# Kernel tuning notes

Hardware: AMD Instinct MI355X
Metric: run time of the kernel (lower is better)

## Reference

```python
import jax, jax.numpy as jnp
import numpy as np

V = 25   # NTU joints
NE = 5   # number of hyper-edge types


def setup_inputs() -> dict:
    key = jax.random.key(0)
    ks = jax.random.split(key, 8)
    N, C, T = 64, 12, 300
    x = jax.random.normal(ks[0], (N, C, T, V), dtype=jnp.float32)
    # binary incidence matrices [V, E] with E == V, as in the NTU hyper-edge tables
    hs = [jax.random.bernoulli(ks[1 + i], 0.2, (V, V)).astype(jnp.float32) for i in range(NE)]
    in_ch, out_ch = 3, 64
    w_mlp = jax.random.normal(ks[6], (out_ch, in_ch * NE), dtype=jnp.float32) * (1.0 / np.sqrt(in_ch * NE))
    b_mlp = jnp.zeros((out_ch,), dtype=jnp.float32)
    return {"x": x, "h_local": hs[0], "h_center": hs[1], "h_figl": hs[2],
            "h_figr": hs[3], "h_hand": hs[4], "w_mlp": w_mlp, "b_mlp": b_mlp}


def _normalized_aggregate(w, h):
    # w: [N, T, E], h: [V, E] (E == V)
    degree_v = jnp.einsum('ve,bte->btv', h, w)
    # pow(d, -0.5): inf at d==0 and nan at d<0 are both zeroed in the original
    dv_pos = degree_v > 0
    degree_v = jnp.where(dv_pos, jax.lax.rsqrt(jnp.where(dv_pos, degree_v, 1.0)), 0.0)
    degree_e = jnp.sum(h, axis=0)                      # [E]
    de_nz = degree_e != 0
    degree_e = jnp.where(de_nz, 1.0 / jnp.where(de_nz, degree_e, 1.0), 0.0)
    # fused dh * w * degree_e chain: [N, T, V, E]
    dhwb = degree_v[..., None] * h[None, None] * w[:, :, None, :] * degree_e
    dhwbht = jnp.einsum('btve,ue->btvu', dhwb, h)      # [N, T, V, V]
    return dhwbht * degree_v[:, :, None, :]


def reference(x, h_local, h_center, h_figl, h_figr, h_hand, w_mlp, b_mlp):
    ws = (x[:, 6], x[:, 7], x[:, 9], x[:, 10], x[:, 11])
    hs = (h_local, h_center, h_figl, h_figr, h_hand)
    hwh_cat = jnp.concatenate([_normalized_aggregate(w, h) for w, h in zip(ws, hs)], axis=-2)  # [N,T,5V,V]
    feat = x[:, :3]                                    # [N, 3, T, V]
    N, C, T, Vv = feat.shape
    support = jnp.einsum('btvu,bctu->bctv', hwh_cat, feat)          # [N, C, T, 5V]
    support = support.reshape(N, C, T, NE, Vv).transpose(0, 3, 1, 2, 4).reshape(N, NE * C, T, Vv)
    out = jnp.einsum('oi,bitv->botv', w_mlp, support) + b_mlp[None, :, None, None]
    return jax.nn.relu(out)
```

## Files before the change

### kernel.cpp

```cpp
#include <hip/hip_runtime.h>

#define NE  5
#define V   25
#define NT  300
#define NC  12
#define CO  64
#define WPB 4
#define GX  38

typedef float f4 __attribute__((ext_vector_type(4)));
typedef float f2 __attribute__((ext_vector_type(2)));

#define WSYNC() do { asm volatile("s_waitcnt lgkmcnt(0)" ::: "memory"); \
                     __builtin_amdgcn_sched_barrier(0); } while (0)

__device__ __forceinline__ float hsel(unsigned m, int e, float w) {
    int s = ((int)(m << (31 - e))) >> 31;
    return __int_as_float(__float_as_int(w) & s);
}

#define OW   0
#define ODV  224
#define OG   364
#define OB   504
#define OFP  924
#define OST  1344
#define SCRF 2344

__global__ __launch_bounds__(256, 4) void hyper_main(
    const float* __restrict__ x,
    const float* __restrict__ h0, const float* __restrict__ h1,
    const float* __restrict__ h2, const float* __restrict__ h3,
    const float* __restrict__ h4,
    const float* __restrict__ wmlp, const float* __restrict__ bmlp,
    float* __restrict__ out)
{
    __shared__ unsigned RM[125];
    __shared__ unsigned CM[125];
    __shared__ float    DE[125];
    __shared__ __align__(16) float SCR[WPB][SCRF];

    const int tid  = threadIdx.x;
    const int lane = tid & 63;
    const int wid  = tid >> 6;
    const int b    = blockIdx.y;

    if (tid < 125) {
        int i = tid / 25, v = tid % 25;
        const float* hp = (i==0)?h0:(i==1)?h1:(i==2)?h2:(i==3)?h3:h4;
        unsigned m = 0;
        for (int e = 0; e < V; ++e) if (hp[v*V + e] != 0.f) m |= (1u << e);
        RM[tid] = m;
    } else if (tid < 250) {
        int idx = tid - 125, i = idx / 25, e = idx % 25;
        const float* hp = (i==0)?h0:(i==1)?h1:(i==2)?h2:(i==3)?h3:h4;
        unsigned m = 0; float s = 0.f;
        for (int u = 0; u < V; ++u) {
            float hv = hp[u*V + e];
            s += hv;
            if (hv != 0.f) m |= (1u << u);
        }
        CM[idx] = m;
        DE[idx] = (s != 0.f) ? __fdiv_rn(1.f, s) : 0.f;
    }
    __syncthreads();

    const int pp = blockIdx.x * WPB + wid;
    if (pp >= NT/2) return;

    float* S = SCR[wid];

    const float* xb[4]; int lo[4];
    {
        #pragma unroll
        for (int r = 0; r < 4; ++r) {
            int q  = r*64 + lane;
            int qq = (q < 200) ? q : 0;
            int ch = qq / 25, e = qq % 25;
            int xc = (ch < 5) ? (ch + 6 + (ch >= 2 ? 1 : 0)) : (ch - 5);
            lo[r] = OW + ch*28 + e;
            xb[r] = x + (size_t)(b*NC + xc)*NT*V + e;
        }
    }
    const bool act3 = (lane < 8);

    float pf0, pf1, pf2, pf3;
    {
        int t0 = 2 * pp;
        pf0 = xb[0][t0*V]; pf1 = xb[1][t0*V];
        pf2 = xb[2][t0*V]; pf3 = xb[3][t0*V];
    }

    for (int tp = 0; tp < 2; ++tp) {

        S[lo[0]] = pf0; S[lo[1]] = pf1; S[lo[2]] = pf2;
        if (act3) S[lo[3]] = pf3;
        WSYNC();

        if (tp == 0) {
            int tn = 2*pp + 1;
            pf0 = xb[0][tn*V]; pf1 = xb[1][tn*V];
            pf2 = xb[2][tn*V]; pf3 = xb[3][tn*V];
        }

        for (int r = 0; r < 2; ++r) {
            int idx = r*64 + lane;
            if (idx < 125) {
                int i = idx / 25, v = idx % 25;
                unsigned m = RM[idx];
                const float* wi = S + OW + i*28;
                f4 w0 = *(const f4*)(wi+0),  w1 = *(const f4*)(wi+4),
                   w2 = *(const f4*)(wi+8),  w3 = *(const f4*)(wi+12),
                   w4 = *(const f4*)(wi+16), w5 = *(const f4*)(wi+20),
                   w6 = *(const f4*)(wi+24);
                float L0 = 0.f, L1 = 0.f, L2 = 0.f, L3 = 0.f;
                L0=__fadd_rn(L0,hsel(m, 0,w0.x)); L1=__fadd_rn(L1,hsel(m, 1,w0.y));
                L2=__fadd_rn(L2,hsel(m, 2,w0.z)); L3=__fadd_rn(L3,hsel(m, 3,w0.w));
                L0=__fadd_rn(L0,hsel(m, 4,w1.x)); L1=__fadd_rn(L1,hsel(m, 5,w1.y));
                L2=__fadd_rn(L2,hsel(m, 6,w1.z)); L3=__fadd_rn(L3,hsel(m, 7,w1.w));
                L0=__fadd_rn(L0,hsel(m, 8,w2.x)); L1=__fadd_rn(L1,hsel(m, 9,w2.y));
                L2=__fadd_rn(L2,hsel(m,10,w2.z)); L3=__fadd_rn(L3,hsel(m,11,w2.w));
                L0=__fadd_rn(L0,hsel(m,12,w3.x)); L1=__fadd_rn(L1,hsel(m,13,w3.y));
                L2=__fadd_rn(L2,hsel(m,14,w3.z)); L3=__fadd_rn(L3,hsel(m,15,w3.w));
                L0=__fadd_rn(L0,hsel(m,16,w4.x)); L1=__fadd_rn(L1,hsel(m,17,w4.y));
                L2=__fadd_rn(L2,hsel(m,18,w4.z)); L3=__fadd_rn(L3,hsel(m,19,w4.w));
                L0=__fadd_rn(L0,hsel(m,20,w5.x)); L1=__fadd_rn(L1,hsel(m,21,w5.y));
                L2=__fadd_rn(L2,hsel(m,22,w5.z)); L3=__fadd_rn(L3,hsel(m,23,w5.w));
                float s = __fadd_rn(__fadd_rn(L0,L1), __fadd_rn(L2,L3));
                s = __fadd_rn(s, hsel(m, 24, w6.x));
                float dvv = (s > 0.f) ? (float)(1.0 / sqrt((double)s)) : 0.f;
                S[ODV + i*28 + v] = dvv;
                S[OG  + i*28 + v] = S[OW + i*28 + v] * DE[idx];
                float f0 = S[OW + 5*28 + v];
                float f1 = S[OW + 6*28 + v];
                float f2v = S[OW + 7*28 + v];
                S[OB + (0*5+i)*28 + v] = dvv * f0;
                S[OB + (1*5+i)*28 + v] = dvv * f1;
                S[OB + (2*5+i)*28 + v] = dvv * f2v;
            }
        }
        WSYNC();

        for (int r = 0; r < 2; ++r) {
            int idx = r*64 + lane;
            if (idx < 125) {
                int i = idx / 25, e = idx % 25;
                unsigned m = CM[idx];
                const float* bp = S + OB + i*28;
                float a0 = 0.f, a1 = 0.f, a2 = 0.f;
                while (m) {
                    int u = __builtin_ctz(m); m &= m - 1;
                    a0 += bp[u]; a1 += bp[140 + u]; a2 += bp[280 + u];
                }
                float gg = S[OG + i*28 + e];
                S[OFP + (i*3+0)*28 + e] = a0 * gg;
                S[OFP + (i*3+1)*28 + e] = a1 * gg;
                S[OFP + (i*3+2)*28 + e] = a2 * gg;
            }
        }
        WSYNC();

        for (int r = 0; r < 2; ++r) {
            int idx = r*64 + lane;
            if (idx < 125) {
                int i = idx / 25, v = idx % 25;
                unsigned m = RM[idx];
                const float* fp = S + OFP + i*3*28;
                float a0 = 0.f, a1 = 0.f, a2 = 0.f;
                while (m) {
                    int e = __builtin_ctz(m); m &= m - 1;
                    a0 += fp[e]; a1 += fp[28 + e]; a2 += fp[56 + e];
                }
                float dd = S[ODV + i*28 + v];
                float* st = S + OST + (tp*25 + v)*20 + i*3;
                st[0] = a0 * dd; st[1] = a1 * dd; st[2] = a2 * dd;
            }
        }
        WSYNC();
    }

    if (lane < 50) {
        const float* st = S + OST + lane*20;
        f4 s0 = *(const f4*)(st+0), s1 = *(const f4*)(st+4),
           s2 = *(const f4*)(st+8), s3 = *(const f4*)(st+12);
        s3.w = 0.f;
        float* ob = out + (size_t)b*CO*7500 + (size_t)pp*50 + lane;
        #pragma unroll 2
        for (int o2 = 0; o2 < 32; ++o2) {
            int o = 2*o2;
            const float* wa = wmlp + o*15;
            const float* wb = wa + 15;
            f2 a = (f2){bmlp[o], bmlp[o+1]};
            a += (f2){wa[ 0], wb[ 0]} * s0.x;
            a += (f2){wa[ 1], wb[ 1]} * s0.y;
            a += (f2){wa[ 2], wb[ 2]} * s0.z;
            a += (f2){wa[ 3], wb[ 3]} * s0.w;
            a += (f2){wa[ 4], wb[ 4]} * s1.x;
            a += (f2){wa[ 5], wb[ 5]} * s1.y;
            a += (f2){wa[ 6], wb[ 6]} * s1.z;
            a += (f2){wa[ 7], wb[ 7]} * s1.w;
            a += (f2){wa[ 8], wb[ 8]} * s2.x;
            a += (f2){wa[ 9], wb[ 9]} * s2.y;
            a += (f2){wa[10], wb[10]} * s2.z;
            a += (f2){wa[11], wb[11]} * s2.w;
            a += (f2){wa[12], wb[12]} * s3.x;
            a += (f2){wa[13], wb[13]} * s3.y;
            a += (f2){wa[14], wb[14]} * s3.z;
            __builtin_nontemporal_store(fmaxf(a.x, 0.f), ob + (size_t)o*7500);
            __builtin_nontemporal_store(fmaxf(a.y, 0.f), ob + (size_t)(o+1)*7500);
        }
    }
}

extern "C" void kernel_launch(void* const* d_in, const int* in_sizes, int n_in,
                              void* d_out, int out_size, void* d_ws, size_t ws_size,
                              hipStream_t stream) {
    const float* x    = (const float*)d_in[0];
    const float* h0   = (const float*)d_in[1];
    const float* h1   = (const float*)d_in[2];
    const float* h2   = (const float*)d_in[3];
    const float* h3   = (const float*)d_in[4];
    const float* h4   = (const float*)d_in[5];
    const float* wmlp = (const float*)d_in[6];
    const float* bmlp = (const float*)d_in[7];
    float* out = (float*)d_out;

    hyper_main<<<dim3(GX, 64, 1), dim3(256,1,1), 0, stream>>>(
        x, h0, h1, h2, h3, h4, wmlp, bmlp, out);
}
```

Before: 76.16 us.

## Process both timesteps of a wave together in one pass

Each wave now loads both timesteps' inputs up front and runs each aggregation stage once over 250 work items, instead of looping twice over 125 items. This halves the number of in-wave LDS sync points and fills nearly all lanes in each stage iteration. The separate gated-weight buffer is dropped: that product is recomputed where it is needed. The scratch layout now lets the output staging area alias regions that are dead by then, and the per-wave scratch grows slightly. The trade-off is that the software prefetch overlap between timesteps is lost, and the larger LDS footprint may affect occupancy.

```diff
diff --git a/kernel.cpp b/kernel.cpp
--- a/kernel.cpp
+++ b/kernel.cpp
@@ -19,13 +19,12 @@
     return __int_as_float(__float_as_int(w) & s);
 }
 
-#define OW   0
-#define ODV  224
-#define OG   364
-#define OB   504
-#define OFP  924
-#define OST  1344
-#define SCRF 2344
+#define ODV  0
+#define OFP  280
+#define OWB  1120
+#define OBB  1568
+#define OST  1408
+#define SCRF 2408
 
 __global__ __launch_bounds__(256, 4) void hyper_main(
     const float* __restrict__ x,
@@ -70,114 +69,103 @@
 
     float* S = SCR[wid];
 
-    const float* xb[4]; int lo[4];
-    {
-        #pragma unroll
-        for (int r = 0; r < 4; ++r) {
-            int q  = r*64 + lane;
-            int qq = (q < 200) ? q : 0;
-            int ch = qq / 25, e = qq % 25;
-            int xc = (ch < 5) ? (ch + 6 + (ch >= 2 ? 1 : 0)) : (ch - 5);
-            lo[r] = OW + ch*28 + e;
-            xb[r] = x + (size_t)(b*NC + xc)*NT*V + e;
-        }
-    }
-    const bool act3 = (lane < 8);
-
-    float pf0, pf1, pf2, pf3;
-    {
-        int t0 = 2 * pp;
-        pf0 = xb[0][t0*V]; pf1 = xb[1][t0*V];
-        pf2 = xb[2][t0*V]; pf3 = xb[3][t0*V];
-    }
-
-    for (int tp = 0; tp < 2; ++tp) {
-
-        S[lo[0]] = pf0; S[lo[1]] = pf1; S[lo[2]] = pf2;
-        if (act3) S[lo[3]] = pf3;
-        WSYNC();
-
-        if (tp == 0) {
-            int tn = 2*pp + 1;
-            pf0 = xb[0][tn*V]; pf1 = xb[1][tn*V];
-            pf2 = xb[2][tn*V]; pf3 = xb[3][tn*V];
-        }
-
-        for (int r = 0; r < 2; ++r) {
-            int idx = r*64 + lane;
-            if (idx < 125) {
-                int i = idx / 25, v = idx % 25;
-                unsigned m = RM[idx];
-                const float* wi = S + OW + i*28;
-                f4 w0 = *(const f4*)(wi+0),  w1 = *(const f4*)(wi+4),
-                   w2 = *(const f4*)(wi+8),  w3 = *(const f4*)(wi+12),
-                   w4 = *(const f4*)(wi+16), w5 = *(const f4*)(wi+20),
-                   w6 = *(const f4*)(wi+24);
-                float L0 = 0.f, L1 = 0.f, L2 = 0.f, L3 = 0.f;
-                L0=__fadd_rn(L0,hsel(m, 0,w0.x)); L1=__fadd_rn(L1,hsel(m, 1,w0.y));
-                L2=__fadd_rn(L2,hsel(m, 2,w0.z)); L3=__fadd_rn(L3,hsel(m, 3,w0.w));
-                L0=__fadd_rn(L0,hsel(m, 4,w1.x)); L1=__fadd_rn(L1,hsel(m, 5,w1.y));
-                L2=__fadd_rn(L2,hsel(m, 6,w1.z)); L3=__fadd_rn(L3,hsel(m, 7,w1.w));
-                L0=__fadd_rn(L0,hsel(m, 8,w2.x)); L1=__fadd_rn(L1,hsel(m, 9,w2.y));
-                L2=__fadd_rn(L2,hsel(m,10,w2.z)); L3=__fadd_rn(L3,hsel(m,11,w2.w));
-                L0=__fadd_rn(L0,hsel(m,12,w3.x)); L1=__fadd_rn(L1,hsel(m,13,w3.y));
-                L2=__fadd_rn(L2,hsel(m,14,w3.z)); L3=__fadd_rn(L3,hsel(m,15,w3.w));
-                L0=__fadd_rn(L0,hsel(m,16,w4.x)); L1=__fadd_rn(L1,hsel(m,17,w4.y));
-                L2=__fadd_rn(L2,hsel(m,18,w4.z)); L3=__fadd_rn(L3,hsel(m,19,w4.w));
-                L0=__fadd_rn(L0,hsel(m,20,w5.x)); L1=__fadd_rn(L1,hsel(m,21,w5.y));
-                L2=__fadd_rn(L2,hsel(m,22,w5.z)); L3=__fadd_rn(L3,hsel(m,23,w5.w));
-                float s = __fadd_rn(__fadd_rn(L0,L1), __fadd_rn(L2,L3));
-                s = __fadd_rn(s, hsel(m, 24, w6.x));
-                float dvv = (s > 0.f) ? (float)(1.0 / sqrt((double)s)) : 0.f;
-                S[ODV + i*28 + v] = dvv;
-                S[OG  + i*28 + v] = S[OW + i*28 + v] * DE[idx];
-                float f0 = S[OW + 5*28 + v];
-                float f1 = S[OW + 6*28 + v];
-                float f2v = S[OW + 7*28 + v];
-                S[OB + (0*5+i)*28 + v] = dvv * f0;
-                S[OB + (1*5+i)*28 + v] = dvv * f1;
-                S[OB + (2*5+i)*28 + v] = dvv * f2v;
+    float pf[7]; int lo[7];
+    #pragma unroll
+    for (int r = 0; r < 7; ++r) {
+        int q  = r*64 + lane;
+        int qq = (q < 400) ? q : 0;
+        int tt = qq / 200, rr = qq % 200, ch = rr / 25, e = rr % 25;
+        int xc = (ch < 5) ? (ch + 6 + (ch >= 2 ? 1 : 0)) : (ch - 5);
+        lo[r] = OWB + tt*224 + ch*28 + e;
+        pf[r] = x[((size_t)(b*NC + xc)*NT + (2*pp + tt))*V + e];
+    }
+    #pragma unroll
+    for (int r = 0; r < 6; ++r) S[lo[r]] = pf[r];
+    if (lane < 16) S[lo[6]] = pf[6];
+    WSYNC();
+
+    #pragma unroll
+    for (int r = 0; r < 4; ++r) {
+        int idx = r*64 + lane;
+        if (idx < 250) {
+            int tt  = (idx >= 125) ? 1 : 0;
+            int rem = idx - (tt ? 125 : 0);
+            int i = rem / 25, v = rem % 25;
+            unsigned m = RM[rem];
+            const float* wi = S + OWB + tt*224 + i*28;
+            f4 w0 = *(const f4*)(wi+0),  w1 = *(const f4*)(wi+4),
+               w2 = *(const f4*)(wi+8),  w3 = *(const f4*)(wi+12),
+               w4 = *(const f4*)(wi+16), w5 = *(const f4*)(wi+20),
+               w6 = *(const f4*)(wi+24);
+            float L0 = 0.f, L1 = 0.f, L2 = 0.f, L3 = 0.f;
+            L0=__fadd_rn(L0,hsel(m, 0,w0.x)); L1=__fadd_rn(L1,hsel(m, 1,w0.y));
+            L2=__fadd_rn(L2,hsel(m, 2,w0.z)); L3=__fadd_rn(L3,hsel(m, 3,w0.w));
+            L0=__fadd_rn(L0,hsel(m, 4,w1.x)); L1=__fadd_rn(L1,hsel(m, 5,w1.y));
+            L2=__fadd_rn(L2,hsel(m, 6,w1.z)); L3=__fadd_rn(L3,hsel(m, 7,w1.w));
+            L0=__fadd_rn(L0,hsel(m, 8,w2.x)); L1=__fadd_rn(L1,hsel(m, 9,w2.y));
+            L2=__fadd_rn(L2,hsel(m,10,w2.z)); L3=__fadd_rn(L3,hsel(m,11,w2.w));
+            L0=__fadd_rn(L0,hsel(m,12,w3.x)); L1=__fadd_rn(L1,hsel(m,13,w3.y));
+            L2=__fadd_rn(L2,hsel(m,14,w3.z)); L3=__fadd_rn(L3,hsel(m,15,w3.w));
+            L0=__fadd_rn(L0,hsel(m,16,w4.x)); L1=__fadd_rn(L1,hsel(m,17,w4.y));
+            L2=__fadd_rn(L2,hsel(m,18,w4.z)); L3=__fadd_rn(L3,hsel(m,19,w4.w));
+            L0=__fadd_rn(L0,hsel(m,20,w5.x)); L1=__fadd_rn(L1,hsel(m,21,w5.y));
+            L2=__fadd_rn(L2,hsel(m,22,w5.z)); L3=__fadd_rn(L3,hsel(m,23,w5.w));
+            float s = __fadd_rn(__fadd_rn(L0,L1), __fadd_rn(L2,L3));
+            s = __fadd_rn(s, hsel(m, 24, w6.x));
+            float dvv = (s > 0.f) ? (float)(1.0 / sqrt((double)s)) : 0.f;
+            S[ODV + tt*140 + i*28 + v] = dvv;
+            float f0  = S[OWB + tt*224 + 5*28 + v];
+            float f1  = S[OWB + tt*224 + 6*28 + v];
+            float f2v = S[OWB + tt*224 + 7*28 + v];
+            S[OBB + tt*420 + (0*5+i)*28 + v] = dvv * f0;
+            S[OBB + tt*420 + (1*5+i)*28 + v] = dvv * f1;
+            S[OBB + tt*420 + (2*5+i)*28 + v] = dvv * f2v;
+        }
+    }
+    WSYNC();
+
+    #pragma unroll
+    for (int r = 0; r < 4; ++r) {
+        int idx = r*64 + lane;
+        if (idx < 250) {
+            int tt  = (idx >= 125) ? 1 : 0;
+            int rem = idx - (tt ? 125 : 0);
+            int i = rem / 25, e = rem % 25;
+            unsigned m = CM[rem];
+            const float* bp = S + OBB + tt*420 + i*28;
+            float a0 = 0.f, a1 = 0.f, a2 = 0.f;
+            while (m) {
+                int u = __builtin_ctz(m); m &= m - 1;
+                a0 += bp[u]; a1 += bp[140 + u]; a2 += bp[280 + u];
             }
-        }
-        WSYNC();
-
-        for (int r = 0; r < 2; ++r) {
-            int idx = r*64 + lane;
-            if (idx < 125) {
-                int i = idx / 25, e = idx % 25;
-                unsigned m = CM[idx];
-                const float* bp = S + OB + i*28;
-                float a0 = 0.f, a1 = 0.f, a2 = 0.f;
-                while (m) {
-                    int u = __builtin_ctz(m); m &= m - 1;
-                    a0 += bp[u]; a1 += bp[140 + u]; a2 += bp[280 + u];
-                }
-                float gg = S[OG + i*28 + e];
-                S[OFP + (i*3+0)*28 + e] = a0 * gg;
-                S[OFP + (i*3+1)*28 + e] = a1 * gg;
-                S[OFP + (i*3+2)*28 + e] = a2 * gg;
+            float gg = S[OWB + tt*224 + i*28 + e] * DE[rem];
+            S[OFP + tt*420 + (i*3+0)*28 + e] = a0 * gg;
+            S[OFP + tt*420 + (i*3+1)*28 + e] = a1 * gg;
+            S[OFP + tt*420 + (i*3+2)*28 + e] = a2 * gg;
+        }
+    }
+    WSYNC();
+
+    #pragma unroll
+    for (int r = 0; r < 4; ++r) {
+        int idx = r*64 + lane;
+        if (idx < 250) {
+            int tt  = (idx >= 125) ? 1 : 0;
+            int rem = idx - (tt ? 125 : 0);
+            int i = rem / 25, v = rem % 25;
+            unsigned m = RM[rem];
+            const float* fp = S + OFP + tt*420 + i*3*28;
+            float a0 = 0.f, a1 = 0.f, a2 = 0.f;
+            while (m) {
+                int e = __builtin_ctz(m); m &= m - 1;
+                a0 += fp[e]; a1 += fp[28 + e]; a2 += fp[56 + e];
             }
-        }
-        WSYNC();
-
-        for (int r = 0; r < 2; ++r) {
-            int idx = r*64 + lane;
-            if (idx < 125) {
-                int i = idx / 25, v = idx % 25;
-                unsigned m = RM[idx];
-                const float* fp = S + OFP + i*3*28;
-                float a0 = 0.f, a1 = 0.f, a2 = 0.f;
-                while (m) {
-                    int e = __builtin_ctz(m); m &= m - 1;
-                    a0 += fp[e]; a1 += fp[28 + e]; a2 += fp[56 + e];
-                }
-                float dd = S[ODV + i*28 + v];
-                float* st = S + OST + (tp*25 + v)*20 + i*3;
-                st[0] = a0 * dd; st[1] = a1 * dd; st[2] = a2 * dd;
-            }
-        }
-        WSYNC();
-    }
+            float dd = S[ODV + tt*140 + i*28 + v];
+            float* st = S + OST + (tt*25 + v)*20 + i*3;
+            st[0] = a0 * dd; st[1] = a1 * dd; st[2] = a2 * dd;
+        }
+    }
+    WSYNC();
 
     if (lane < 50) {
         const float* st = S + OST + lane*20;
```

Result: no change. 76.11 us (-0.1%).
